# Kernel tuning notes

Hardware: AMD Instinct MI355X
Metric: run time of the kernel (lower is better)

## Reference

```python
import jax, jax.numpy as jnp
import numpy as np
from jax import lax

DATA, WIDTH, BATCH, T = 64, 256, 512, 16
MAX_SUBSTEPS = 8
RTOL, ATOL, SAFETY, FMIN, FMAX = 1e-3, 1e-6, 0.9, 0.2, 10.0

# Tsit5 Butcher tableau (Tsitouras 2011), autonomous field so c-nodes unused.
A21 = 0.161
A31, A32 = -0.008480655492356989, 0.335480655492357
A41, A42, A43 = 2.8971530571054935, -6.359448489975075, 4.3622954328695815
A51, A52, A53, A54 = 5.325864828439257, -11.748883564062828, 7.4955393428898365, -0.09249506636175525
A61, A62, A63, A64, A65 = 5.86145544294642, -12.92096931784711, 8.159367898576159, -0.071584973281401, -0.028269050394068383
B1, B2, B3, B4, B5, B6 = 0.09646076681806523, 0.01, 0.4798896504144996, 1.379008574103742, -3.290069515436081, 2.324710524099774
E1, E2, E3, E4, E5, E6, E7 = -0.001780011052226, -0.000816434459657, 0.007880878010262, -0.144711007173263, 0.582357165452555, -0.458082105929187, 0.015151515151515152


def setup_inputs() -> dict:
    key = jax.random.key(0)
    ks = jax.random.split(key, 4)
    ts = jnp.linspace(0.0, 1.0, T, dtype=jnp.float32)
    y0 = jax.random.normal(ks[0], (BATCH, DATA), dtype=jnp.float32)
    s_in = 1.0 / np.sqrt(DATA)
    s_w = 1.0 / np.sqrt(WIDTH)
    W0 = jax.random.normal(ks[1], (WIDTH, DATA), dtype=jnp.float32) * s_in
    b0 = jnp.zeros((WIDTH,), dtype=jnp.float32)
    W1 = jax.random.normal(ks[2], (WIDTH, WIDTH), dtype=jnp.float32) * s_w
    b1 = jnp.zeros((WIDTH,), dtype=jnp.float32)
    W2 = jax.random.normal(ks[3], (DATA, WIDTH), dtype=jnp.float32) * s_w
    b2 = jnp.zeros((DATA,), dtype=jnp.float32)
    return {"ts": ts, "y0": y0, "W0": W0, "b0": b0, "W1": W1, "b1": b1, "W2": W2, "b2": b2}


def _mlp(y, W0, b0, W1, b1, W2, b2):
    h = jax.nn.softplus(W0 @ y + b0)
    h = jax.nn.softplus(W1 @ h + b1)
    return W2 @ h + b2


def _tsit5_step(f, y, dt):
    k1 = f(y)
    k2 = f(y + dt * (A21 * k1))
    k3 = f(y + dt * (A31 * k1 + A32 * k2))
    k4 = f(y + dt * (A41 * k1 + A42 * k2 + A43 * k3))
    k5 = f(y + dt * (A51 * k1 + A52 * k2 + A53 * k3 + A54 * k4))
    k6 = f(y + dt * (A61 * k1 + A62 * k2 + A63 * k3 + A64 * k4 + A65 * k5))
    y_new = y + dt * (B1 * k1 + B2 * k2 + B3 * k3 + B4 * k4 + B5 * k5 + B6 * k6)
    k7 = f(y_new)  # FSAL stage, used only in the embedded error estimate here
    err = dt * (E1 * k1 + E2 * k2 + E3 * k3 + E4 * k4 + E5 * k5 + E6 * k6 + E7 * k7)
    return y_new, err


def _solve(ts, y0, Wb):
    f = lambda y: _mlp(y, *Wb)
    dt0 = ts[1] - ts[0]
    pairs = jnp.stack([ts[:-1], ts[1:]], axis=1)  # [T-1, 2]

    def interval(carry, pair):
        y, dt = carry
        t0, t1 = pair[0], pair[1]

        def substep(c, _):
            t, y, dt = c
            rem = t1 - t
            done = rem <= 1e-6
            dt_c = jnp.where(done, dt, jnp.minimum(dt, rem))
            y_new, err = _tsit5_step(f, y, dt_c)
            scale = ATOL + RTOL * jnp.maximum(jnp.abs(y), jnp.abs(y_new))
            err_norm = jnp.sqrt(jnp.mean((err / scale) ** 2))
            accept = err_norm <= 1.0
            # integral (I) controller, order-5 method -> exponent -1/5
            factor = jnp.clip(SAFETY * jnp.maximum(err_norm, 1e-10) ** (-0.2), FMIN, FMAX)
            step = jnp.logical_and(accept, jnp.logical_not(done))
            t_n = jnp.where(step, t + dt_c, t)
            y_n = jnp.where(step, y_new, y)
            dt_n = jnp.where(done, dt, dt_c * factor)
            return (t_n, y_n, dt_n), None

        (_, yF, dtF), _ = lax.scan(substep, (t0, y, dt), None, length=MAX_SUBSTEPS)
        return (yF, dtF), yF

    _, ys_tail = lax.scan(interval, (y0, dt0), pairs)
    return jnp.concatenate([y0[None], ys_tail], axis=0)  # [T, DATA]


def reference(ts, y0, W0, b0, W1, b1, W2, b2):
    Wb = (W0, b0, W1, b1, W2, b2)
    return jax.vmap(lambda y: _solve(ts, y, Wb))(y0)  # [BATCH, T, DATA]
```

## Files before the change

### kernel.cpp

```cpp
#include <hip/hip_runtime.h>
#include <math.h>

#define DATA 64
#define WIDTH 256
#define BATCHN 512
#define TPTS 16
#define MAXSUB 8
#define NSAMP 2
#define NBLK (BATCHN / NSAMP)
#define NTHR 1024

#define RTOLc 1e-3f
#define ATOLc 1e-6f
#define SAFETYc 0.9f
#define FMINc 0.2f
#define FMAXc 10.0f

#define A21 0.161f
#define A31 (-0.008480655492356989f)
#define A32 0.335480655492357f
#define A41 2.8971530571054935f
#define A42 (-6.359448489975075f)
#define A43 4.3622954328695815f
#define A51 5.325864828439257f
#define A52 (-11.748883564062828f)
#define A53 7.4955393428898365f
#define A54 (-0.09249506636175525f)
#define A61 5.86145544294642f
#define A62 (-12.92096931784711f)
#define A63 8.159367898576159f
#define A64 (-0.071584973281401f)
#define A65 (-0.028269050394068383f)
#define B1c 0.09646076681806523f
#define B2c 0.01f
#define B3c 0.4798896504144996f
#define B4c 1.379008574103742f
#define B5c (-3.290069515436081f)
#define B6c 2.324710524099774f
#define E1c (-0.001780011052226f)
#define E2c (-0.000816434459657f)
#define E3c 0.007880878010262f
#define E4c (-0.144711007173263f)
#define E5c 0.582357165452555f
#define E6c (-0.458082105929187f)
#define E7c 0.015151515151515152f

__device__ __forceinline__ float softplus_jax(float x) {
    return fmaxf(x, 0.0f) + log1pf(expf(-fabsf(x)));
}

#define DOT4(acc, wq, xv)                                                     \
    acc = fmaf((wq).x, (xv).x, acc); acc = fmaf((wq).y, (xv).y, acc);         \
    acc = fmaf((wq).z, (xv).z, acc); acc = fmaf((wq).w, (xv).w, acc);

#define FEVAL_CORE(PIN0, PIN1)                                                \
    {                                                            \
        const float* x0 = (PIN0) + h * 16;                                    \
        const float* x1 = (PIN1) + h * 16;                                    \
        float a0 = 0.f, a1 = 0.f;                                             \
        _Pragma("unroll")                                                     \
        for (int kk = 0; kk < 16; ++kk) {                                     \
            const float w = sW0T[h * 16 + kk][r];                             \
            a0 = fmaf(w, x0[kk], a0); a1 = fmaf(w, x1[kk], a1);               \
        }                                                                     \
        s_ps[0][h][r] = a0; s_ps[1][h][r] = a1;                               \
    }                                                                         \
    __syncthreads();                                                          \
    if (t < 512) {                                                            \
        const int s = t >> 8;                                                 \
        s_h0[s][r] = softplus_jax(((s_ps[s][0][r] + s_ps[s][1][r])            \
                                 + (s_ps[s][2][r] + s_ps[s][3][r])) + b0r);   \
    }                                                                         \
    __syncthreads();                                                          \
    {                                                            \
        const float4* x0 = reinterpret_cast<const float4*>(&s_h0[0][h * 64]); \
        const float4* x1 = reinterpret_cast<const float4*>(&s_h0[1][h * 64]); \
        float a0 = 0.f, a1 = 0.f, c0 = 0.f, c1 = 0.f;                         \
        _Pragma("unroll")                                                     \
        for (int j = 0; j < 16; j += 2) {                                     \
            float4 u = x0[j], v = x1[j];                                      \
            DOT4(a0, w1q[j], u); DOT4(a1, w1q[j], v);                         \
            float4 u2 = x0[j + 1], v2 = x1[j + 1];                            \
            DOT4(c0, w1q[j + 1], u2); DOT4(c1, w1q[j + 1], v2);               \
        }                                                                     \
        s_ps[0][h][r] = a0 + c0; s_ps[1][h][r] = a1 + c1;                     \
    }                                                                         \
    __syncthreads();                                                          \
    if (t < 512) {                                                            \
        const int s = t >> 8;                                                 \
        s_h1[s][r] = softplus_jax(((s_ps[s][0][r] + s_ps[s][1][r])            \
                                 + (s_ps[s][2][r] + s_ps[s][3][r])) + b1r);   \
    }                                                                         \
    __syncthreads();                                                          \
    {                                                            \
        const float* x0 = &s_h1[0][kc * 16];                                  \
        const float* x1 = &s_h1[1][kc * 16];                                  \
        float a0 = 0.f, a1 = 0.f;                                             \
        _Pragma("unroll")                                                     \
        for (int kk = 0; kk < 16; ++kk) {                                     \
            const float w = sW2T[kc * 16 + kk][d];                            \
            a0 = fmaf(w, x0[kk], a0); a1 = fmaf(w, x1[kk], a1);               \
        }                                                                     \
        s_ps2[0][kc][d] = a0; s_ps2[1][kc][d] = a1;                           \
    }                                                                         \
    __syncthreads();

#define KV_SUM(s)                                                             \
    (((((s_ps2[s][0][d] + s_ps2[s][1][d]) + (s_ps2[s][2][d] + s_ps2[s][3][d]))  \
     + ((s_ps2[s][4][d] + s_ps2[s][5][d]) + (s_ps2[s][6][d] + s_ps2[s][7][d]))) \
    + (((s_ps2[s][8][d] + s_ps2[s][9][d]) + (s_ps2[s][10][d] + s_ps2[s][11][d]))\
     + ((s_ps2[s][12][d] + s_ps2[s][13][d]) + (s_ps2[s][14][d] + s_ps2[s][15][d])))) \
    + b2d)

__global__ __launch_bounds__(NTHR)
void ode_kernel(const float* __restrict__ ts, const float* __restrict__ y0,
                const float* __restrict__ W0, const float* __restrict__ b0,
                const float* __restrict__ W1, const float* __restrict__ b1,
                const float* __restrict__ W2, const float* __restrict__ b2,
                float* __restrict__ out)
{
    __shared__ __align__(16) float sW0T[DATA][WIDTH];
    __shared__ __align__(16) float sW2T[WIDTH][DATA];
    __shared__ __align__(16) float s_ps[NSAMP][4][WIDTH];
    __shared__ __align__(16) float s_ps2[NSAMP][16][DATA];
    __shared__ __align__(16) float s_h0[NSAMP][WIDTH];
    __shared__ __align__(16) float s_h1[NSAMP][WIDTH];
    __shared__ __align__(16) float s_y[NSAMP][DATA];
    __shared__ __align__(16) float s_yst[NSAMP][DATA];
    __shared__ __align__(16) float s_ynew[NSAMP][DATA];
    __shared__ __align__(16) float s_k[NSAMP][6][DATA];
    __shared__ float s_err[NSAMP];

    const int t  = threadIdx.x;
    const int r  = t & 255;
    const int h  = t >> 8;
    const int d  = t & 63;
    const int kc = t >> 6;
    const int b  = blockIdx.x;

    float4 w1q[16];
    {
        const float4* p1 = reinterpret_cast<const float4*>(W1 + r * WIDTH + h * 64);
#pragma unroll
        for (int j = 0; j < 16; ++j) w1q[j] = p1[j];
    }
    for (int i = t; i < DATA * WIDTH; i += NTHR) {
        const int rr = i >> 6, kk = i & 63;
        sW0T[kk][rr] = W0[i];
    }
    for (int i = t; i < DATA * WIDTH; i += NTHR) {
        const int dd = i >> 8, kk = i & 255;
        sW2T[kk][dd] = W2[i];
    }
    const float b0r = b0[r];
    const float b1r = b1[r];
    const float b2d = b2[d];
    if (t < NSAMP * DATA) {
        const int s = t >> 6;
        const float v = y0[(b * NSAMP + s) * DATA + d];
        s_y[s][d] = v;
        out[(size_t)(b * NSAMP + s) * TPTS * DATA + d] = v;
    }
    __syncthreads();

    float dtv0 = ts[1] - ts[0];
    float dtv1 = dtv0;

    for (int iv = 0; iv < TPTS - 1; ++iv) {
        const float t1v = ts[iv + 1];
        float tc0 = ts[iv], tc1 = tc0;

        for (int ss = 0; ss < MAXSUB; ++ss) {
            const float rem0 = t1v - tc0, rem1 = t1v - tc1;
            const bool done0 = rem0 <= 1e-6f, done1 = rem1 <= 1e-6f;
            if (done0 && done1) break;
            const float dtc0 = done0 ? dtv0 : fminf(dtv0, rem0);
            const float dtc1 = done1 ? dtv1 : fminf(dtv1, rem1);

            FEVAL_CORE(&s_y[0][0], &s_y[1][0])
            if (t < 128) {
                const int s = t >> 6;
                const float dtc_s = (s == 0) ? dtc0 : dtc1;
                const float kv = KV_SUM(s);
                s_k[s][0][d] = kv;
                s_yst[s][d] = s_y[s][d] + dtc_s * (A21 * kv);
            }
            __syncthreads();
            FEVAL_CORE(&s_yst[0][0], &s_yst[1][0])
            if (t < 128) {
                const int s = t >> 6;
                const float dtc_s = (s == 0) ? dtc0 : dtc1;
                const float kv = KV_SUM(s);
                s_k[s][1][d] = kv;
                s_yst[s][d] = s_y[s][d] + dtc_s * (A31 * s_k[s][0][d] + A32 * kv);
            }
            __syncthreads();
            FEVAL_CORE(&s_yst[0][0], &s_yst[1][0])
            if (t < 128) {
                const int s = t >> 6;
                const float dtc_s = (s == 0) ? dtc0 : dtc1;
                const float kv = KV_SUM(s);
                s_k[s][2][d] = kv;
                s_yst[s][d] = s_y[s][d] + dtc_s * (A41 * s_k[s][0][d] + A42 * s_k[s][1][d] + A43 * kv);
            }
            __syncthreads();
            FEVAL_CORE(&s_yst[0][0], &s_yst[1][0])
            if (t < 128) {
                const int s = t >> 6;
                const float dtc_s = (s == 0) ? dtc0 : dtc1;
                const float kv = KV_SUM(s);
                s_k[s][3][d] = kv;
                s_yst[s][d] = s_y[s][d] + dtc_s * (A51 * s_k[s][0][d] + A52 * s_k[s][1][d]
                                                 + A53 * s_k[s][2][d] + A54 * kv);
            }
            __syncthreads();
            FEVAL_CORE(&s_yst[0][0], &s_yst[1][0])
            if (t < 128) {
                const int s = t >> 6;
                const float dtc_s = (s == 0) ? dtc0 : dtc1;
                const float kv = KV_SUM(s);
                s_k[s][4][d] = kv;
                s_yst[s][d] = s_y[s][d] + dtc_s * (A61 * s_k[s][0][d] + A62 * s_k[s][1][d]
                                                 + A63 * s_k[s][2][d] + A64 * s_k[s][3][d] + A65 * kv);
            }
            __syncthreads();
            FEVAL_CORE(&s_yst[0][0], &s_yst[1][0])
            if (t < 128) {
                const int s = t >> 6;
                const float dtc_s = (s == 0) ? dtc0 : dtc1;
                const float kv = KV_SUM(s);
                s_k[s][5][d] = kv;
                s_ynew[s][d] = s_y[s][d] + dtc_s * (B1c * s_k[s][0][d] + B2c * s_k[s][1][d]
                                                  + B3c * s_k[s][2][d] + B4c * s_k[s][3][d]
                                                  + B5c * s_k[s][4][d] + B6c * kv);
            }
            __syncthreads();
            FEVAL_CORE(&s_ynew[0][0], &s_ynew[1][0])
            if (t < 128) {
                const int s = t >> 6;
                const float dtc_s = (s == 0) ? dtc0 : dtc1;
                const float kv = KV_SUM(s);
                const float e = dtc_s * (E1c * s_k[s][0][d] + E2c * s_k[s][1][d]
                                       + E3c * s_k[s][2][d] + E4c * s_k[s][3][d]
                                       + E5c * s_k[s][4][d] + E6c * s_k[s][5][d] + E7c * kv);
                const float yv = s_y[s][d], ynv = s_ynew[s][d];
                const float sc = ATOLc + RTOLc * fmaxf(fabsf(yv), fabsf(ynv));
                const float rr2 = e / sc;
                float v = rr2 * rr2;
#pragma unroll
                for (int off = 32; off > 0; off >>= 1) v += __shfl_xor(v, off, 64);
                if (d == 0) s_err[s] = v;
            }
            __syncthreads();

            const float en0 = sqrtf(s_err[0] * (1.0f / DATA));
            const float en1 = sqrtf(s_err[1] * (1.0f / DATA));
            const bool acc0 = en0 <= 1.0f, acc1 = en1 <= 1.0f;
            float f0 = fminf(fmaxf(SAFETYc * powf(fmaxf(en0, 1e-10f), -0.2f), FMINc), FMAXc);
            float f1 = fminf(fmaxf(SAFETYc * powf(fmaxf(en1, 1e-10f), -0.2f), FMINc), FMAXc);
            const bool step0 = acc0 && !done0, step1 = acc1 && !done1;
            if (t < 128) {
                const int s = t >> 6;
                const bool st = (s == 0) ? step0 : step1;
                if (st) s_y[s][d] = s_ynew[s][d];
            }
            if (step0) tc0 += dtc0;
            if (step1) tc1 += dtc1;
            dtv0 = done0 ? dtv0 : dtc0 * f0;
            dtv1 = done1 ? dtv1 : dtc1 * f1;
            __syncthreads();
        }

        if (t < 128) {
            const int s = t >> 6;
            out[(size_t)(b * NSAMP + s) * TPTS * DATA + (size_t)(iv + 1) * DATA + d] = s_y[s][d];
        }
    }
}

extern "C" void kernel_launch(void* const* d_in, const int* in_sizes, int n_in,
                              void* d_out, int out_size, void* d_ws, size_t ws_size,
                              hipStream_t stream)
{
    const float* ts = (const float*)d_in[0];
    const float* y0 = (const float*)d_in[1];
    const float* W0 = (const float*)d_in[2];
    const float* b0 = (const float*)d_in[3];
    const float* W1 = (const float*)d_in[4];
    const float* b1 = (const float*)d_in[5];
    const float* W2 = (const float*)d_in[6];
    const float* b2 = (const float*)d_in[7];
    float* out = (float*)d_out;

    ode_kernel<<<NBLK, NTHR, 0, stream>>>(ts, y0, W0, b0, W1, b1, W2, b2, out);
}
```

Measured before the change: 469.2 us.

## Register-block MLP layers as 4-output outer products with W2 held in registers

Restructures all three MLP matvecs so each thread computes four output rows via float4 outer-product FMAs over a 16-way split of the reduction dimension. W0 is stored packed as float4 in shared memory, W1 is held transposed in registers, and W2 moves from shared memory into registers, which removes the sW2T array. Softplus reductions now run on 128 threads with 16-way partial sums, and biases and ts are staged in shared memory. The aim is fewer shared-memory loads per FMA, at the cost of more registers, a larger s_ps4 partial-sum buffer and a longer serial reduction on fewer threads.

```diff
diff --git a/kernel.cpp b/kernel.cpp
--- a/kernel.cpp
+++ b/kernel.cpp
@@ -49,59 +49,81 @@
     return fmaxf(x, 0.0f) + log1pf(expf(-fabsf(x)));
 }
 
-#define DOT4(acc, wq, xv)                                                     \
-    acc = fmaf((wq).x, (xv).x, acc); acc = fmaf((wq).y, (xv).y, acc);         \
-    acc = fmaf((wq).z, (xv).z, acc); acc = fmaf((wq).w, (xv).w, acc);
+__device__ __forceinline__ float4 f4add(const float4 a, const float4 b) {
+    float4 r; r.x = a.x + b.x; r.y = a.y + b.y; r.z = a.z + b.z; r.w = a.w + b.w; return r;
+}
+
+#define FMA4(a, w, xs)                                                        \
+    a.x = fmaf((w).x, (xs), a.x); a.y = fmaf((w).y, (xs), a.y);               \
+    a.z = fmaf((w).z, (xs), a.z); a.w = fmaf((w).w, (xs), a.w);
+
+#define PSUM16(P, gg)                                                         \
+    f4add(f4add(f4add(f4add(P[0][gg],  P[1][gg]),  f4add(P[2][gg],  P[3][gg])),  \
+                f4add(f4add(P[4][gg],  P[5][gg]),  f4add(P[6][gg],  P[7][gg]))), \
+          f4add(f4add(f4add(P[8][gg],  P[9][gg]),  f4add(P[10][gg], P[11][gg])), \
+                f4add(f4add(P[12][gg], P[13][gg]), f4add(P[14][gg], P[15][gg]))))
 
 #define FEVAL_CORE(PIN0, PIN1)                                                \
-    {                                                            \
-        const float* x0 = (PIN0) + h * 16;                                    \
-        const float* x1 = (PIN1) + h * 16;                                    \
-        float a0 = 0.f, a1 = 0.f;                                             \
+    {                                                        \
+        const float4 x0 = *reinterpret_cast<const float4*>((PIN0) + c4);      \
+        const float4 x1 = *reinterpret_cast<const float4*>((PIN1) + c4);      \
+        float4 a0 = {0,0,0,0}, a1 = {0,0,0,0};                                \
+        float4 w;                                                             \
+        w = sW0p[c4 + 0][g]; FMA4(a0, w, x0.x) FMA4(a1, w, x1.x)              \
+        w = sW0p[c4 + 1][g]; FMA4(a0, w, x0.y) FMA4(a1, w, x1.y)              \
+        w = sW0p[c4 + 2][g]; FMA4(a0, w, x0.z) FMA4(a1, w, x1.z)              \
+        w = sW0p[c4 + 3][g]; FMA4(a0, w, x0.w) FMA4(a1, w, x1.w)              \
+        s_ps4[0][c][g] = a0; s_ps4[1][c][g] = a1;                             \
+    }                                                                         \
+    __syncthreads();                                                          \
+    if (t < 128) {             \
+        const int s = t >> 6, gg = t & 63;                                    \
+        const float4 acc = PSUM16(s_ps4[s], gg);                              \
+        s_h0[s][gg]       = softplus_jax(acc.x + s_b0[gg]);                   \
+        s_h0[s][gg +  64] = softplus_jax(acc.y + s_b0[gg +  64]);             \
+        s_h0[s][gg + 128] = softplus_jax(acc.z + s_b0[gg + 128]);             \
+        s_h0[s][gg + 192] = softplus_jax(acc.w + s_b0[gg + 192]);             \
+    }                                                                         \
+    __syncthreads();                                                          \
+    {                                                        \
+        const float4* xx0 = reinterpret_cast<const float4*>(&s_h0[0][c16]);   \
+        const float4* xx1 = reinterpret_cast<const float4*>(&s_h0[1][c16]);   \
+        float4 a0 = {0,0,0,0}, a1 = {0,0,0,0};                                \
+        float4 w;                                                             \
         _Pragma("unroll")                                                     \
-        for (int kk = 0; kk < 16; ++kk) {                                     \
-            const float w = sW0T[h * 16 + kk][r];                             \
-            a0 = fmaf(w, x0[kk], a0); a1 = fmaf(w, x1[kk], a1);               \
+        for (int j = 0; j < 4; ++j) {                                         \
+            const float4 q0 = xx0[j], q1 = xx1[j];                            \
+            w = w1q[4*j + 0]; FMA4(a0, w, q0.x) FMA4(a1, w, q1.x)             \
+            w = w1q[4*j + 1]; FMA4(a0, w, q0.y) FMA4(a1, w, q1.y)             \
+            w = w1q[4*j + 2]; FMA4(a0, w, q0.z) FMA4(a1, w, q1.z)             \
+            w = w1q[4*j + 3]; FMA4(a0, w, q0.w) FMA4(a1, w, q1.w)             \
         }                                                                     \
-        s_ps[0][h][r] = a0; s_ps[1][h][r] = a1;                               \
+        s_ps4[0][c][g] = a0; s_ps4[1][c][g] = a1;                             \
     }                                                                         \
     __syncthreads();                                                          \
-    if (t < 512) {                                                            \
-        const int s = t >> 8;                                                 \
-        s_h0[s][r] = softplus_jax(((s_ps[s][0][r] + s_ps[s][1][r])            \
-                                 + (s_ps[s][2][r] + s_ps[s][3][r])) + b0r);   \
+    if (t < 128) {                                            \
+        const int s = t >> 6, gg = t & 63;                                    \
+        const float4 acc = PSUM16(s_ps4[s], gg);                              \
+        s_h1[s][gg]       = softplus_jax(acc.x + s_b1[gg]);                   \
+        s_h1[s][gg +  64] = softplus_jax(acc.y + s_b1[gg +  64]);             \
+        s_h1[s][gg + 128] = softplus_jax(acc.z + s_b1[gg + 128]);             \
+        s_h1[s][gg + 192] = softplus_jax(acc.w + s_b1[gg + 192]);             \
     }                                                                         \
     __syncthreads();                                                          \
-    {                                                            \
-        const float4* x0 = reinterpret_cast<const float4*>(&s_h0[0][h * 64]); \
-        const float4* x1 = reinterpret_cast<const float4*>(&s_h0[1][h * 64]); \
-        float a0 = 0.f, a1 = 0.f, c0 = 0.f, c1 = 0.f;                         \
+    {                \
+        const float4* xx0 = reinterpret_cast<const float4*>(&s_h1[0][c16]);   \
+        const float4* xx1 = reinterpret_cast<const float4*>(&s_h1[1][c16]);   \
+        float e0 = 0.f, e1 = 0.f, f0 = 0.f, f1 = 0.f;                         \
         _Pragma("unroll")                                                     \
-        for (int j = 0; j < 16; j += 2) {                                     \
-            float4 u = x0[j], v = x1[j];                                      \
-            DOT4(a0, w1q[j], u); DOT4(a1, w1q[j], v);                         \
-            float4 u2 = x0[j + 1], v2 = x1[j + 1];                            \
-            DOT4(c0, w1q[j + 1], u2); DOT4(c1, w1q[j + 1], v2);               \
+        for (int j = 0; j < 4; ++j) {                                         \
+            const float4 q0 = xx0[j], q1 = xx1[j];                            \
+            const float4 w = w2q[j];                                          \
+            e0 = fmaf(w.x, q0.x, e0); e0 = fmaf(w.y, q0.y, e0);               \
+            f0 = fmaf(w.z, q0.z, f0); f0 = fmaf(w.w, q0.w, f0);               \
+            e1 = fmaf(w.x, q1.x, e1); e1 = fmaf(w.y, q1.y, e1);               \
+            f1 = fmaf(w.z, q1.z, f1); f1 = fmaf(w.w, q1.w, f1);               \
         }                                                                     \
-        s_ps[0][h][r] = a0 + c0; s_ps[1][h][r] = a1 + c1;                     \
-    }                                                                         \
-    __syncthreads();                                                          \
-    if (t < 512) {                                                            \
-        const int s = t >> 8;                                                 \
-        s_h1[s][r] = softplus_jax(((s_ps[s][0][r] + s_ps[s][1][r])            \
-                                 + (s_ps[s][2][r] + s_ps[s][3][r])) + b1r);   \
-    }                                                                         \
-    __syncthreads();                                                          \
-    {                                                            \
-        const float* x0 = &s_h1[0][kc * 16];                                  \
-        const float* x1 = &s_h1[1][kc * 16];                                  \
-        float a0 = 0.f, a1 = 0.f;                                             \
-        _Pragma("unroll")                                                     \
-        for (int kk = 0; kk < 16; ++kk) {                                     \
-            const float w = sW2T[kc * 16 + kk][d];                            \
-            a0 = fmaf(w, x0[kk], a0); a1 = fmaf(w, x1[kk], a1);               \
-        }                                                                     \
-        s_ps2[0][kc][d] = a0; s_ps2[1][kc][d] = a1;                           \
+        s_ps2[0][c][g] = e0 + f0; s_ps2[1][c][g] = e1 + f1;                   \
     }                                                                         \
     __syncthreads();
 
@@ -110,7 +132,7 @@
      + ((s_ps2[s][4][d] + s_ps2[s][5][d]) + (s_ps2[s][6][d] + s_ps2[s][7][d]))) \
     + (((s_ps2[s][8][d] + s_ps2[s][9][d]) + (s_ps2[s][10][d] + s_ps2[s][11][d]))\
      + ((s_ps2[s][12][d] + s_ps2[s][13][d]) + (s_ps2[s][14][d] + s_ps2[s][15][d])))) \
-    + b2d)
+    + s_b2[d])
 
 __global__ __launch_bounds__(NTHR)
 void ode_kernel(const float* __restrict__ ts, const float* __restrict__ y0,
@@ -119,42 +141,60 @@
                 const float* __restrict__ W2, const float* __restrict__ b2,
                 float* __restrict__ out)
 {
-    __shared__ __align__(16) float sW0T[DATA][WIDTH];
-    __shared__ __align__(16) float sW2T[WIDTH][DATA];
-    __shared__ __align__(16) float s_ps[NSAMP][4][WIDTH];
-    __shared__ __align__(16) float s_ps2[NSAMP][16][DATA];
-    __shared__ __align__(16) float s_h0[NSAMP][WIDTH];
-    __shared__ __align__(16) float s_h1[NSAMP][WIDTH];
-    __shared__ __align__(16) float s_y[NSAMP][DATA];
-    __shared__ __align__(16) float s_yst[NSAMP][DATA];
-    __shared__ __align__(16) float s_ynew[NSAMP][DATA];
-    __shared__ __align__(16) float s_k[NSAMP][6][DATA];
+    __shared__ __align__(16) float4 sW0p[DATA][64];
+    __shared__ __align__(16) float4 s_ps4[NSAMP][16][64];
+    __shared__ __align__(16) float  s_ps2[NSAMP][16][DATA];
+    __shared__ __align__(16) float  s_h0[NSAMP][WIDTH];
+    __shared__ __align__(16) float  s_h1[NSAMP][WIDTH];
+    __shared__ __align__(16) float  s_y[NSAMP][DATA];
+    __shared__ __align__(16) float  s_yst[NSAMP][DATA];
+    __shared__ __align__(16) float  s_ynew[NSAMP][DATA];
+    __shared__ __align__(16) float  s_k[NSAMP][6][DATA];
+    __shared__ float s_b0[WIDTH], s_b1[WIDTH], s_b2[DATA];
+    __shared__ float s_ts[TPTS];
     __shared__ float s_err[NSAMP];
 
-    const int t  = threadIdx.x;
-    const int r  = t & 255;
-    const int h  = t >> 8;
-    const int d  = t & 63;
-    const int kc = t >> 6;
-    const int b  = blockIdx.x;
+    const int t   = threadIdx.x;
+    const int g   = t & 63;
+    const int c   = t >> 6;
+    const int c4  = c * 4;
+    const int c16 = c * 16;
+    const int d   = t & 63;
+    const int b   = blockIdx.x;
 
     float4 w1q[16];
     {
-        const float4* p1 = reinterpret_cast<const float4*>(W1 + r * WIDTH + h * 64);
+        const float4* r0 = reinterpret_cast<const float4*>(W1 + (g      ) * WIDTH + c16);
+        const float4* r1 = reinterpret_cast<const float4*>(W1 + (g +  64) * WIDTH + c16);
+        const float4* r2 = reinterpret_cast<const float4*>(W1 + (g + 128) * WIDTH + c16);
+        const float4* r3 = reinterpret_cast<const float4*>(W1 + (g + 192) * WIDTH + c16);
 #pragma unroll
-        for (int j = 0; j < 16; ++j) w1q[j] = p1[j];
-    }
-    for (int i = t; i < DATA * WIDTH; i += NTHR) {
-        const int rr = i >> 6, kk = i & 63;
-        sW0T[kk][rr] = W0[i];
-    }
-    for (int i = t; i < DATA * WIDTH; i += NTHR) {
-        const int dd = i >> 8, kk = i & 255;
-        sW2T[kk][dd] = W2[i];
-    }
-    const float b0r = b0[r];
-    const float b1r = b1[r];
-    const float b2d = b2[d];
+        for (int j = 0; j < 4; ++j) {
+            const float4 q0 = r0[j], q1 = r1[j], q2 = r2[j], q3 = r3[j];
+            w1q[4*j + 0] = make_float4(q0.x, q1.x, q2.x, q3.x);
+            w1q[4*j + 1] = make_float4(q0.y, q1.y, q2.y, q3.y);
+            w1q[4*j + 2] = make_float4(q0.z, q1.z, q2.z, q3.z);
+            w1q[4*j + 3] = make_float4(q0.w, q1.w, q2.w, q3.w);
+        }
+    }
+    float4 w2q[4];
+    {
+        const float4* r2p = reinterpret_cast<const float4*>(W2 + g * WIDTH + c16);
+#pragma unroll
+        for (int j = 0; j < 4; ++j) w2q[j] = r2p[j];
+    }
+    for (int i = t; i < DATA * DATA; i += NTHR) {
+        const int kk = i >> 6, gg = i & 63;
+        float4 w;
+        w.x = W0[(gg      ) * DATA + kk];
+        w.y = W0[(gg +  64) * DATA + kk];
+        w.z = W0[(gg + 128) * DATA + kk];
+        w.w = W0[(gg + 192) * DATA + kk];
+        sW0p[kk][gg] = w;
+    }
+    if (t < WIDTH) { s_b0[t] = b0[t]; s_b1[t] = b1[t]; }
+    if (t < DATA)  { s_b2[t] = b2[t]; }
+    if (t < TPTS)  { s_ts[t] = ts[t]; }
     if (t < NSAMP * DATA) {
         const int s = t >> 6;
         const float v = y0[(b * NSAMP + s) * DATA + d];
@@ -163,12 +203,12 @@
     }
     __syncthreads();
 
-    float dtv0 = ts[1] - ts[0];
+    float dtv0 = s_ts[1] - s_ts[0];
     float dtv1 = dtv0;
 
     for (int iv = 0; iv < TPTS - 1; ++iv) {
-        const float t1v = ts[iv + 1];
-        float tc0 = ts[iv], tc1 = tc0;
+        const float t1v = s_ts[iv + 1];
+        float tc0 = s_ts[iv], tc1 = tc0;
 
         for (int ss = 0; ss < MAXSUB; ++ss) {
             const float rem0 = t1v - tc0, rem1 = t1v - tc1;
```

New measurement: 1.232 ms. +162.6%, slower.
